# Kernel optimization log

Measured on AMD Instinct MI355X. Metric: run time of the kernel, lower is better.

## Reference

```python
import jax, jax.numpy as jnp
import numpy as np

# Standard SMPL kinematic tree (24 joints), parent of joint i
PARENTS = np.array([-1, 0, 0, 0, 1, 2, 3, 4, 5, 6, 7, 8, 9, 9, 9,
                    12, 13, 14, 16, 17, 18, 19, 20, 21])
N_JOINTS = 24
EPS = 1e-8  # stands in for the tiny gaussian eps the torch code adds


def rodrigues(r):
    """Axis-angle (N,3) -> rotation matrices (N,3,3)."""
    theta = jnp.linalg.norm(r, axis=1, keepdims=True) + EPS        # (N,1)
    r_hat = r / theta                                              # (N,3)
    cos = jnp.cos(theta)[..., None]                                # (N,1,1)
    sin = jnp.sin(theta)[..., None]
    z = jnp.zeros_like(r_hat[:, 0])
    # skew-symmetric cross-product matrix of r_hat
    m = jnp.stack([z, -r_hat[:, 2], r_hat[:, 1],
                   r_hat[:, 2], z, -r_hat[:, 0],
                   -r_hat[:, 1], r_hat[:, 0], z], axis=1).reshape(-1, 3, 3)
    outer = r_hat[:, :, None] * r_hat[:, None, :]                  # (N,3,3)
    eye = jnp.eye(3, dtype=r.dtype)
    return cos * eye + (1.0 - cos) * outer + sin * m


def setup_inputs() -> dict:
    key = jax.random.key(0)
    k0, k1, k2, k3, k4 = jax.random.split(key, 5)
    B, V, J = 512, 6890, N_JOINTS
    return {
        "T_hat": jax.random.normal(k0, (V, 3), dtype=jnp.float32),
        "J_hat": jax.random.normal(k1, (J, 3), dtype=jnp.float32),
        "weights": jax.random.uniform(k2, (V, J), dtype=jnp.float32),
        "pose": jax.random.normal(k3, (B, J * 3), dtype=jnp.float32),
        "trans": jax.random.normal(k4, (B, 3), dtype=jnp.float32),
    }


def reference(T_hat, J_hat, weights, pose, trans):
    B = pose.shape[0]
    dt = pose.dtype
    # per-joint rotation matrices: (B,24,3,3)
    R = rodrigues(pose.reshape(-1, 3)).reshape(B, N_JOINTS, 3, 3)

    # relative joint offsets along the tree (24,3)
    rel_J = jnp.concatenate([J_hat[:1], J_hat[1:] - J_hat[PARENTS[1:]]], axis=0)

    # local SE(3) transforms (B,24,4,4)
    top = jnp.concatenate(
        [R, jnp.broadcast_to(rel_J[None, :, :, None], (B, N_JOINTS, 3, 1))],
        axis=-1)                                                   # (B,24,3,4)
    bottom = jnp.broadcast_to(
        jnp.array([0.0, 0.0, 0.0, 1.0], dtype=dt), (B, N_JOINTS, 1, 4))
    G_local = jnp.concatenate([top, bottom], axis=2)               # (B,24,4,4)

    # forward kinematics along the fixed 24-joint tree (small fixed loop)
    results = [G_local[:, 0]]
    for i in range(1, N_JOINTS):
        results.append(jnp.matmul(results[PARENTS[i]], G_local[:, i]))
    G = jnp.stack(results, axis=1)                                 # (B,24,4,4)

    # remove rest-pose joint locations from the translation column
    Jh = jnp.concatenate(
        [J_hat, jnp.zeros((N_JOINTS, 1), dtype=dt)], axis=1)       # (24,4)
    corr = jnp.einsum('bjxy,jy->bjx', G, Jh)                       # (B,24,4)
    G = G.at[:, :, :, 3].add(-corr)

    # linear blend skinning: per-vertex blended transforms (B,V,4,4)
    T = jnp.einsum('bjxy,vj->bvxy', G, weights)
    vh = jnp.concatenate(
        [T_hat, jnp.ones((T_hat.shape[0], 1), dtype=dt)], axis=1)  # (V,4)
    v = jnp.einsum('bvxy,vy->bvx', T, vh)[..., :3]                 # (B,V,3)
    return v + trans[:, None, :]
```

## Files before the change

### kernel.cpp

```cpp
#include <hip/hip_runtime.h>
#include <math.h>

#define NJ 24
#define TPB 256
#define BPT 4
#define FK_BPB 8

typedef _Float16 f16x8 __attribute__((ext_vector_type(8)));
typedef float f32x4 __attribute__((ext_vector_type(4)));

__device__ __constant__ int PAR[NJ] = {-1,0,0,0,1,2,3,4,5,6,7,8,9,9,9,12,13,14,16,17,18,19,20,21};
__device__ __constant__ int CHAIN[NJ][9] = {
  {0,-1,-1,-1,-1,-1,-1,-1,-1},
  {0, 1,-1,-1,-1,-1,-1,-1,-1},
  {0, 2,-1,-1,-1,-1,-1,-1,-1},
  {0, 3,-1,-1,-1,-1,-1,-1,-1},
  {0, 1, 4,-1,-1,-1,-1,-1,-1},
  {0, 2, 5,-1,-1,-1,-1,-1,-1},
  {0, 3, 6,-1,-1,-1,-1,-1,-1},
  {0, 1, 4, 7,-1,-1,-1,-1,-1},
  {0, 2, 5, 8,-1,-1,-1,-1,-1},
  {0, 3, 6, 9,-1,-1,-1,-1,-1},
  {0, 1, 4, 7,10,-1,-1,-1,-1},
  {0, 2, 5, 8,11,-1,-1,-1,-1},
  {0, 3, 6, 9,12,-1,-1,-1,-1},
  {0, 3, 6, 9,13,-1,-1,-1,-1},
  {0, 3, 6, 9,14,-1,-1,-1,-1},
  {0, 3, 6, 9,12,15,-1,-1,-1},
  {0, 3, 6, 9,13,16,-1,-1,-1},
  {0, 3, 6, 9,14,17,-1,-1,-1},
  {0, 3, 6, 9,13,16,18,-1,-1},
  {0, 3, 6, 9,14,17,19,-1,-1},
  {0, 3, 6, 9,13,16,18,20,-1},
  {0, 3, 6, 9,14,17,19,21,-1},
  {0, 3, 6, 9,13,16,18,20,22},
  {0, 3, 6, 9,14,17,19,21,23},
};


__device__ __forceinline__ void fk_local(const float* __restrict__ J_hat,
                                         const float* __restrict__ pose,
                                         int b, int j, float* __restrict__ L )
{
  const float rx = pose[b * 72 + j * 3 + 0];
  const float ry = pose[b * 72 + j * 3 + 1];
  const float rz = pose[b * 72 + j * 3 + 2];
  const float theta = sqrtf(rx * rx + ry * ry + rz * rz) + 1e-8f;
  const float inv = 1.0f / theta;
  const float ux = rx * inv, uy = ry * inv, uz = rz * inv;
  const float c = cosf(theta), s = sinf(theta);
  const float ic = 1.0f - c;

  float tx = J_hat[j * 3 + 0];
  float ty = J_hat[j * 3 + 1];
  float tz = J_hat[j * 3 + 2];
  const int p = PAR[j];
  if (p >= 0) {
    tx -= J_hat[p * 3 + 0];
    ty -= J_hat[p * 3 + 1];
    tz -= J_hat[p * 3 + 2];
  }

  L[0]  = c + ic * ux * ux;
  L[1]  = ic * ux * uy - s * uz;
  L[2]  = ic * ux * uz + s * uy;
  L[3]  = tx;
  L[4]  = ic * uy * ux + s * uz;
  L[5]  = c + ic * uy * uy;
  L[6]  = ic * uy * uz - s * ux;
  L[7]  = ty;
  L[8]  = ic * uz * ux - s * uy;
  L[9]  = ic * uz * uy + s * ux;
  L[10] = c + ic * uz * uz;
  L[11] = tz;
}

__device__ __forceinline__ void fk_compose(const float (*__restrict__ Lc)[12],
                                           const float* __restrict__ J_hat,
                                           int j, float* __restrict__ g )
{
#pragma unroll
  for (int k = 0; k < 12; k++) g[k] = Lc[0][k];
#pragma unroll
  for (int d = 1; d < 9; d++) {
    const int a = CHAIN[j][d];
    if (a >= 0) {
      float l[12];
#pragma unroll
      for (int k = 0; k < 12; k++) l[k] = Lc[a][k];
      float n[12];
#pragma unroll
      for (int r = 0; r < 3; r++) {
        const float gr0 = g[r * 4 + 0], gr1 = g[r * 4 + 1], gr2 = g[r * 4 + 2];
        n[r * 4 + 0] = gr0 * l[0] + gr1 * l[4] + gr2 * l[8];
        n[r * 4 + 1] = gr0 * l[1] + gr1 * l[5] + gr2 * l[9];
        n[r * 4 + 2] = gr0 * l[2] + gr1 * l[6] + gr2 * l[10];
        n[r * 4 + 3] = gr0 * l[3] + gr1 * l[7] + gr2 * l[11] + g[r * 4 + 3];
      }
#pragma unroll
      for (int k = 0; k < 12; k++) g[k] = n[k];
    }
  }
  const float jx = J_hat[j * 3 + 0], jy = J_hat[j * 3 + 1], jz = J_hat[j * 3 + 2];
  g[3]  -= g[0] * jx + g[1] * jy + g[2]  * jz;
  g[7]  -= g[4] * jx + g[5] * jy + g[6]  * jz;
  g[11] -= g[8] * jx + g[9] * jy + g[10] * jz;
}


__global__ __launch_bounds__(TPB) void smpl_prep_all(
    const float* __restrict__ weights,
    const float* __restrict__ J_hat,
    const float* __restrict__ pose,
    _Float16* __restrict__ W_h,
    _Float16* __restrict__ G_hT,
    int V, int VP, int nvchunks, int B)
{
  __shared__ __align__(16) float Lc[FK_BPB][NJ][12];
  const int tid = threadIdx.x;

  if ((int)blockIdx.x < nvchunks) {
    const int v = blockIdx.x * TPB + tid;
    if (v >= VP) return;
    _Float16 row[32];
#pragma unroll
    for (int k = 0; k < 32; k++) row[k] = (_Float16)0.f;
    if (v < V) {
      const float4* wp = reinterpret_cast<const float4*>(weights + (size_t)v * 24);
#pragma unroll
      for (int q = 0; q < 6; q++) {
        const float4 t = wp[q];
        row[q * 4 + 0] = (_Float16)t.x;
        row[q * 4 + 1] = (_Float16)t.y;
        row[q * 4 + 2] = (_Float16)t.z;
        row[q * 4 + 3] = (_Float16)t.w;
      }
    }
    float4* dst = reinterpret_cast<float4*>(W_h + (size_t)v * 32);
    const float4* src = reinterpret_cast<const float4*>(row);
#pragma unroll
    for (int q = 0; q < 4; q++) dst[q] = src[q];
  } else {
    const int lb = tid >> 5;
    const int j  = tid & 31;
    const int b  = (blockIdx.x - nvchunks) * FK_BPB + lb;
    const bool compute = (j < NJ) && (b < B);

    if (compute) {
      float L[12];
      fk_local(J_hat, pose, b, j, L);
#pragma unroll
      for (int k = 0; k < 12; k++) Lc[lb][j][k] = L[k];
    }
    __syncthreads();

    float g[12];
#pragma unroll
    for (int k = 0; k < 12; k++) g[k] = 0.0f;
    if (compute) fk_compose(Lc[lb], J_hat, j, g);

    if (b < B) {
      _Float16* dst = G_hT + (size_t)b * 512;
#pragma unroll
      for (int c = 0; c < 16; c++) {
        _Float16 val = (_Float16)0.f;
        if (j < NJ && c < 12) val = (_Float16)g[c];
        dst[c * 32 + j] = val;
      }
    }
  }
}

__global__ __launch_bounds__(TPB) void smpl_blend_mfma(
    const float* __restrict__ T_hat,
    const _Float16* __restrict__ W_h,
    const float* __restrict__ trans,
    const _Float16* __restrict__ G_hT,
    float* __restrict__ out,
    int V)
{
  const int tid  = threadIdx.x;
  const int wid  = tid >> 6;
  const int lane = tid & 63;
  const int vbase = blockIdx.x * 256 + wid * 64;
  const int b0 = blockIdx.y * BPT;

  const int fr = lane & 15;
  const int kb = lane >> 4;

  f16x8 wfrag[4];
#pragma unroll
  for (int t = 0; t < 4; t++)
    wfrag[t] = *reinterpret_cast<const f16x8*>(
        W_h + ((size_t)(vbase + t * 16 + fr)) * 32 + kb * 8);

  f16x8 gfrag[BPT];
#pragma unroll
  for (int bi = 0; bi < BPT; bi++)
    gfrag[bi] = *reinterpret_cast<const f16x8*>(
        G_hT + ((size_t)(b0 + bi) * 16 + fr) * 32 + kb * 8);

  float thx[4], thy[4], thz[4];
#pragma unroll
  for (int t = 0; t < 4; t++) {
    const int v = vbase + t * 16 + fr;
    if (v < V) {
      thx[t] = T_hat[v * 3 + 0];
      thy[t] = T_hat[v * 3 + 1];
      thz[t] = T_hat[v * 3 + 2];
    } else {
      thx[t] = thy[t] = thz[t] = 0.f;
    }
  }

  const int kc = (kb < 3) ? kb : 2;
  float tsel[BPT];
#pragma unroll
  for (int bi = 0; bi < BPT; bi++) tsel[bi] = trans[(b0 + bi) * 3 + kc];

#pragma unroll
  for (int bi = 0; bi < BPT; bi++) {
    const int b = b0 + bi;
#pragma unroll
    for (int t = 0; t < 4; t++) {
      f32x4 acc = {0.f, 0.f, 0.f, 0.f};
      acc = __builtin_amdgcn_mfma_f32_16x16x32_f16(gfrag[bi], wfrag[t], acc, 0, 0, 0);
      const float o = acc[0] * thx[t] + acc[1] * thy[t] + acc[2] * thz[t]
                    + acc[3] + tsel[bi];
      const int v = vbase + t * 16 + fr;
      if (kb < 3 && v < V)
        out[((size_t)b * V + v) * 3 + kb] = o;
    }
  }
}


__global__ __launch_bounds__(TPB) void smpl_blend_lds_kernel(
    const float* __restrict__ T_hat,
    const float* __restrict__ J_hat,
    const float* __restrict__ weights,
    const float* __restrict__ pose,
    const float* __restrict__ trans,
    float* __restrict__ out, int V)
{
  __shared__ __align__(16) float Lc[NJ][12];
  __shared__ __align__(16) float Gm[NJ][12];
  const int b = blockIdx.y;
  const int tid = threadIdx.x;

  if (tid < NJ) {
    float L[12];
    fk_local(J_hat, pose, b, tid, L);
#pragma unroll
    for (int k = 0; k < 12; k++) Lc[tid][k] = L[k];
  }
  __syncthreads();
  if (tid < NJ) {
    float g[12];
    fk_compose(Lc, J_hat, tid, g);
#pragma unroll
    for (int k = 0; k < 12; k++) Gm[tid][k] = g[k];
  }
  __syncthreads();

  const int v = blockIdx.x * TPB + tid;
  if (v >= V) return;

  float acc[12];
#pragma unroll
  for (int k = 0; k < 12; k++) acc[k] = 0.0f;
  const float* wv = weights + (size_t)v * 24;
#pragma unroll
  for (int j = 0; j < NJ; j++) {
    const float wj = wv[j];
#pragma unroll
    for (int k = 0; k < 12; k++) acc[k] = fmaf(wj, Gm[j][k], acc[k]);
  }
  const float x = T_hat[v * 3 + 0], y = T_hat[v * 3 + 1], z = T_hat[v * 3 + 2];
  float* op = out + ((size_t)b * V + v) * 3;
  op[0] = acc[0] * x + acc[1] * y + acc[2]  * z + acc[3]  + trans[b * 3 + 0];
  op[1] = acc[4] * x + acc[5] * y + acc[6]  * z + acc[7]  + trans[b * 3 + 1];
  op[2] = acc[8] * x + acc[9] * y + acc[10] * z + acc[11] + trans[b * 3 + 2];
}

extern "C" void kernel_launch(void* const* d_in, const int* in_sizes, int n_in,
                              void* d_out, int out_size, void* d_ws, size_t ws_size,
                              hipStream_t stream) {
  const float* T_hat   = (const float*)d_in[0];
  const float* J_hat   = (const float*)d_in[1];
  const float* weights = (const float*)d_in[2];
  const float* pose    = (const float*)d_in[3];
  const float* trans   = (const float*)d_in[4];
  float* out = (float*)d_out;

  const int V = in_sizes[0] / 3;
  const int B = in_sizes[3] / 72;

  const int nvchunks = (V + 255) / 256;
  const int VP = nvchunks * 256;

  const size_t wh_bytes = (size_t)VP * 32 * sizeof(_Float16);
  const size_t gh_bytes = (size_t)B * 512 * sizeof(_Float16);
  const size_t mfma_need = wh_bytes + gh_bytes;

  if (ws_size >= mfma_need && (B % BPT) == 0 && (B % FK_BPB) == 0) {
    _Float16* W_h  = (_Float16*)d_ws;
    _Float16* G_hT = (_Float16*)((char*)d_ws + wh_bytes);

    const int prep_blocks = nvchunks + B / FK_BPB;
    smpl_prep_all<<<prep_blocks, TPB, 0, stream>>>(
        weights, J_hat, pose, W_h, G_hT, V, VP, nvchunks, B);
    dim3 grid(nvchunks, B / BPT);
    smpl_blend_mfma<<<grid, TPB, 0, stream>>>(T_hat, W_h, trans, G_hT, out, V);
  } else {
    dim3 grid(nvchunks, B);
    smpl_blend_lds_kernel<<<grid, TPB, 0, stream>>>(T_hat, J_hat, weights, pose, trans, out, V);
  }
}
```

Baseline: 28.52 us.

## Fuse weight fp16 conversion into blend kernel and double batches per block

The blend kernel now reads the fp32 skinning weights directly and converts them to fp16 MFMA fragments in registers, replacing the separate padded fp16 weight buffer. The prep kernel now only does forward kinematics. Each blend block also handles 8 batch entries instead of 4, so every weight load is reused across more batches and fewer blocks re-read the weights. The cost is more registers per thread for the larger G fragment array, and every block still reads fp32 weights, which is twice the bytes of the old fp16 copy.

Result: no change. 28.07 us (-1.6%).

```diff
diff --git a/kernel.cpp b/kernel.cpp
--- a/kernel.cpp
+++ b/kernel.cpp
@@ -3,7 +3,7 @@
 
 #define NJ 24
 #define TPB 256
-#define BPT 4
+#define BPT 8
 #define FK_BPB 8
 
 typedef _Float16 f16x8 __attribute__((ext_vector_type(8)));
@@ -173,7 +173,7 @@
 
 __global__ __launch_bounds__(TPB) void smpl_blend_mfma(
     const float* __restrict__ T_hat,
-    const _Float16* __restrict__ W_h,
+    const float* __restrict__ weights,
     const float* __restrict__ trans,
     const _Float16* __restrict__ G_hT,
     float* __restrict__ out,
@@ -190,9 +190,19 @@
 
   f16x8 wfrag[4];
 #pragma unroll
-  for (int t = 0; t < 4; t++)
-    wfrag[t] = *reinterpret_cast<const f16x8*>(
-        W_h + ((size_t)(vbase + t * 16 + fr)) * 32 + kb * 8);
+  for (int t = 0; t < 4; t++) {
+    const int v = vbase + t * 16 + fr;
+    f16x8 wf = {};
+    if (kb < 3 && v < V) {
+      const float4* p = reinterpret_cast<const float4*>(weights + (size_t)v * 24 + kb * 8);
+      const float4 a = p[0], c4 = p[1];
+      wf[0] = (_Float16)a.x;  wf[1] = (_Float16)a.y;
+      wf[2] = (_Float16)a.z;  wf[3] = (_Float16)a.w;
+      wf[4] = (_Float16)c4.x; wf[5] = (_Float16)c4.y;
+      wf[6] = (_Float16)c4.z; wf[7] = (_Float16)c4.w;
+    }
+    wfrag[t] = wf;
+  }
 
   f16x8 gfrag[BPT];
 #pragma unroll
@@ -299,21 +309,19 @@
   const int nvchunks = (V + 255) / 256;
   const int VP = nvchunks * 256;
 
-  const size_t wh_bytes = (size_t)VP * 32 * sizeof(_Float16);
   const size_t gh_bytes = (size_t)B * 512 * sizeof(_Float16);
-  const size_t mfma_need = wh_bytes + gh_bytes;
-
-  if (ws_size >= mfma_need && (B % BPT) == 0 && (B % FK_BPB) == 0) {
-    _Float16* W_h  = (_Float16*)d_ws;
-    _Float16* G_hT = (_Float16*)((char*)d_ws + wh_bytes);
-
-    const int prep_blocks = nvchunks + B / FK_BPB;
-    smpl_prep_all<<<prep_blocks, TPB, 0, stream>>>(
-        weights, J_hat, pose, W_h, G_hT, V, VP, nvchunks, B);
+
+  if (ws_size >= gh_bytes && (B % BPT) == 0 && (B % FK_BPB) == 0) {
+    _Float16* G_hT = (_Float16*)d_ws;
+
+    smpl_prep_all<<<B / FK_BPB, TPB, 0, stream>>>(
+        weights, J_hat, pose, G_hT, G_hT, V, VP, 0, B);
     dim3 grid(nvchunks, B / BPT);
-    smpl_blend_mfma<<<grid, TPB, 0, stream>>>(T_hat, W_h, trans, G_hT, out, V);
+    smpl_blend_mfma<<<grid, TPB, 0, stream>>>(
+        T_hat, weights, trans, G_hT, out, V);
   } else {
     dim3 grid(nvchunks, B);
-    smpl_blend_lds_kernel<<<grid, TPB, 0, stream>>>(T_hat, J_hat, weights, pose, trans, out, V);
-  }
-}
+    smpl_blend_lds_kernel<<<grid, TPB, 0, stream>>>(
+        T_hat, J_hat, weights, pose, trans, out, V);
+  }
+}
```
